# Kernel tuning notes

Measured on AMD Instinct MI355X. Metric: run time of the kernel, lower is better.

Reference implementation:

```python
import jax, jax.numpy as jnp
import numpy as np
import math

B, C, IMG, E, H, L, FF, D, NCLS = 4, 3, 64, 256, 8, 512, 4, 4, 1000
N = IMG * IMG  # 4096 pixel tokens
HS = H * E    # head_size = embedding_size * heads (per original code)


def setup_inputs() -> dict:
    key = jax.random.key(0)
    ks = jax.random.split(key, 32)
    s = 0.02
    nrm = lambda k, shape: (jax.random.normal(k, shape, jnp.float32) * s)
    inp = {
        "x": jax.random.normal(ks[0], (B, C, N), jnp.float32),
        "conv_w": nrm(ks[1], (E, C)),                 # 1x1 conv1d kernel
        "conv_b": jnp.zeros((E,), jnp.float32),
        "pos_emb": nrm(ks[2], (N, E)),
        "latents": jax.random.normal(ks[3], (L, E), jnp.float32),
        # cross-attention (queries from latents, keys/values from image tokens)
        "ca_wq": nrm(ks[4], (E, HS)),
        "ca_wk": nrm(ks[5], (E, HS)),
        "ca_wv": nrm(ks[6], (E, HS)),
        "ca_wu": nrm(ks[7], (HS, E)),
        "ca_bu": jnp.zeros((E,), jnp.float32),
        "ca_ln_g": jnp.ones((E,), jnp.float32),
        "ca_ln_b": jnp.zeros((E,), jnp.float32),
        # transformer blocks, stacked along depth for lax.scan
        "blk_wq": nrm(ks[8], (D, E, HS)),
        "blk_wk": nrm(ks[9], (D, E, HS)),
        "blk_wv": nrm(ks[10], (D, E, HS)),
        "blk_wu": nrm(ks[11], (D, HS, E)),
        "blk_bu": jnp.zeros((D, E), jnp.float32),
        "blk_ln1_g": jnp.ones((D, E), jnp.float32),
        "blk_ln1_b": jnp.zeros((D, E), jnp.float32),
        "blk_w1": nrm(ks[12], (D, E, FF * E)),
        "blk_b1": jnp.zeros((D, FF * E), jnp.float32),
        "blk_w2": nrm(ks[13], (D, FF * E, E)),
        "blk_b2": jnp.zeros((D, E), jnp.float32),
        "blk_ln2_g": jnp.ones((D, E), jnp.float32),
        "blk_ln2_b": jnp.zeros((D, E), jnp.float32),
        "cls_w": nrm(ks[14], (E, NCLS)),
        "cls_b": jnp.zeros((NCLS,), jnp.float32),
        "heads": H,
    }
    return inp


def _ln(x, g, b):
    m = jnp.mean(x, axis=-1, keepdims=True)
    v = jnp.mean(jnp.square(x - m), axis=-1, keepdims=True)
    return g * (x - m) * jax.lax.rsqrt(v + 1e-5) + b


def _mha(q_in, kv_in, wq, wk, wv, wu, bu, heads):
    # Faithful to original: each head has dim = embedding_size (head_size = heads*emb),
    # and the scale is sqrt(emb // heads).
    b, nq, e = q_in.shape
    nk = kv_in.shape[1]
    q = (q_in @ wq).reshape(b, nq, heads, e)
    k = (kv_in @ wk).reshape(b, nk, heads, e)
    v = (kv_in @ wv).reshape(b, nk, heads, e)
    scale = 1.0 / math.sqrt(e // heads)
    w = jax.nn.softmax(jnp.einsum('bqhe,bkhe->bhqk', q, k) * scale, axis=-1)
    a = jnp.einsum('bhqk,bkhe->bqhe', w, v).reshape(b, nq, heads * e)
    return a @ wu + bu


def reference(x, conv_w, conv_b, pos_emb, latents,
              ca_wq, ca_wk, ca_wv, ca_wu, ca_bu, ca_ln_g, ca_ln_b,
              blk_wq, blk_wk, blk_wv, blk_wu, blk_bu,
              blk_ln1_g, blk_ln1_b, blk_w1, blk_b1, blk_w2, blk_b2,
              blk_ln2_g, blk_ln2_b, cls_w, cls_b, heads):
    bsz = x.shape[0]
    # 1x1 conv1d over flattened pixels: (B, C, N) -> (B, N, E), plus positions
    tokens = jnp.einsum('bcn,ec->bne', x, conv_w) + conv_b + pos_emb
    # latents as queries, image tokens as keys/values (cross-attention)
    z = jnp.broadcast_to(latents, (bsz,) + latents.shape)
    z = _ln(_mha(z, tokens, ca_wq, ca_wk, ca_wv, ca_wu, ca_bu, heads) + z,
            ca_ln_g, ca_ln_b)
    # dropout is identity in eval mode

    def block(z, p):
        wq, wk, wv, wu, bu, g1, b1, w1, c1, w2, c2, g2, b2 = p
        z = _ln(_mha(z, z, wq, wk, wv, wu, bu, heads) + z, g1, b1)
        h = jax.nn.gelu(z @ w1 + c1, approximate=False) @ w2 + c2
        z = _ln(h + z, g2, b2)
        return z, None

    z, _ = jax.lax.scan(block, z,
                        (blk_wq, blk_wk, blk_wv, blk_wu, blk_bu,
                         blk_ln1_g, blk_ln1_b, blk_w1, blk_b1,
                         blk_w2, blk_b2, blk_ln2_g, blk_ln2_b))
    # global average over latents, then classifier
    return jnp.mean(z, axis=1) @ cls_w + cls_b
```

## Files before the change

kernel.cpp:

```cpp
#include <hip/hip_runtime.h>
#include <hip/hip_bf16.h>
#include <math.h>


typedef __attribute__((ext_vector_type(8))) short s8v;
typedef __attribute__((ext_vector_type(4))) float f32x4;
typedef __attribute__((ext_vector_type(16))) float f32x16;
typedef __attribute__((ext_vector_type(4))) unsigned u32x4;

__device__ __forceinline__ short f2b(float f) {
  union { float f; unsigned u; } a; a.f = f;
  unsigned r = a.u + 0x7fff + ((a.u >> 16) & 1);
  return (short)(r >> 16);
}
__device__ __forceinline__ float b2f(short s) {
  union { unsigned u; float f; } a; a.u = ((unsigned)(unsigned short)s) << 16;
  return a.f;
}
__device__ __forceinline__ unsigned cvtpk(float lo, float hi) {
  unsigned r;
  asm("v_cvt_pk_bf16_f32 %0, %1, %2" : "=v"(r) : "v"(lo), "v"(hi));
  return r;
}

__device__ __forceinline__ void gl16(const void* gp, void* lp) {
  __builtin_amdgcn_global_load_lds(
      (const __attribute__((address_space(1))) unsigned int*)gp,
      (__attribute__((address_space(3))) unsigned int*)lp, 16, 0, 0);
}

__global__ __launch_bounds__(256) void k_tokens(
    const float* __restrict__ x, const float* __restrict__ cw,
    const float* __restrict__ cb, const float* __restrict__ pe,
    short* __restrict__ tok)
{
  int idx = blockIdx.x * 256 + threadIdx.x;
  int e = idx & 255;
  int n = (idx >> 8) & 4095;
  int b = idx >> 20;
  float s = cb[e] + pe[n * 256 + e];
#pragma unroll
  for (int c = 0; c < 3; ++c)
    s += x[b * 12288 + c * 4096 + n] * cw[e * 3 + c];
  tok[idx] = f2b(s);
}

template<typename TI>
__global__ __launch_bounds__(256) void k_tr(
    const TI* __restrict__ in, short* __restrict__ out,
    int R, int C, long sIn, long sOut)
{
  __shared__ float t[32][33];
  const TI* ib = in + (long)blockIdx.z * sIn;
  short* ob = out + (long)blockIdx.z * sOut;
  int c0 = blockIdx.x * 32, r0 = blockIdx.y * 32;
  int tx = threadIdx.x & 31, ty = threadIdx.x >> 5;
#pragma unroll
  for (int i = 0; i < 4; ++i)
    t[ty * 4 + i][tx] = (float)ib[(long)(r0 + ty * 4 + i) * C + c0 + tx];
  __syncthreads();
#pragma unroll
  for (int i = 0; i < 4; ++i)
    ob[(long)(c0 + ty * 4 + i) * R + r0 + tx] = f2b(t[tx][ty * 4 + i]);
}

struct TrJob {
  const float* src; short* dst;
  int R, C; long sIn, sOut;
  int mode, tilesPerZ, z, tileBase;
  float scale;
};
struct TrJobs { TrJob j[11]; };

__global__ __launch_bounds__(256) void k_trbatch(TrJobs jb, int njobs)
{
  __shared__ float t[32][33];
  int tb = blockIdx.x, ji = 0;
#pragma unroll
  for (int k = 1; k < 11; ++k)
    if (k < njobs && tb >= jb.j[k].tileBase) ji = k;
  TrJob J = jb.j[ji];
  int local = tb - J.tileBase;
  if (J.mode == 1) {
    long o = (long)local * 8192 + threadIdx.x;
#pragma unroll
    for (int k = 0; k < 32; ++k)
      J.dst[o + k * 256] = f2b(J.src[o + k * 256] * J.scale);
    return;
  }
  int zi = local / J.tilesPerZ, ti = local - zi * J.tilesPerZ;
  int ntx = J.C >> 5;
  int tx = ti % ntx, ty = ti / ntx;
  const float* ib = J.src + (long)zi * J.sIn;
  short* ob = J.dst + (long)zi * J.sOut;
  int c0 = tx * 32, r0 = ty * 32;
  int lx = threadIdx.x & 31, ly = threadIdx.x >> 5;
#pragma unroll
  for (int i = 0; i < 4; ++i)
    t[ly * 4 + i][lx] = ib[(long)(r0 + ly * 4 + i) * J.C + c0 + lx];
  __syncthreads();
#pragma unroll
  for (int i = 0; i < 4; ++i)
    ob[(long)(c0 + ly * 4 + i) * J.R + r0 + lx] = f2b(t[lx][ly * 4 + i] * J.scale);
}

template<int EPI>
__global__ __launch_bounds__(256) void k_mgemm(
    const short* __restrict__ A, const short* __restrict__ Bt,
    void* __restrict__ Cv, const float* __restrict__ bias,
    int K, int lda, int ldb, int ldc,
    long sA, long sB, long sC, int zdA, int zmA, int zdB, int zmB)
{
  __shared__ char As[8192];
  __shared__ char Bs[8192];
  int z = blockIdx.z;
  const short* Ab = A + ((long)((z / zdA) % zmA)) * sA;
  const short* Bb = Bt + ((long)((z / zdB) % zmB)) * sB;
  int t = threadIdx.x;
  int lane = t & 63, w = t >> 6;
  int wr = w >> 1, wc = w & 1;
  int g = lane >> 4, l15 = lane & 15;
  long row0 = (long)blockIdx.y * 128, col0 = (long)blockIdx.x * 128;
  const f32x4 zz = {0.f, 0.f, 0.f, 0.f};
  f32x4 acc[4][4];
#pragma unroll
  for (int m = 0; m < 4; ++m)
#pragma unroll
    for (int n = 0; n < 4; ++n) acc[m][n] = zz;

  auto mload = [&](s8v* aa, s8v* bb, int kk) {
#pragma unroll
    for (int i = 0; i < 2; ++i) {
      int r = i * 64 + (t >> 2), c = t & 3;
      aa[i] = *(const s8v*)&Ab[(row0 + r) * (long)lda + kk + c * 8];
      bb[i] = *(const s8v*)&Bb[(col0 + r) * (long)ldb + kk + c * 8];
    }
  };
  auto mstore = [&](s8v* aa, s8v* bb) {
#pragma unroll
    for (int i = 0; i < 2; ++i) {
      int r = i * 64 + (t >> 2), c = t & 3;
      int off = (r * 64 + c * 16) ^ ((r & 7) << 4);
      *(s8v*)&As[off] = aa[i];
      *(s8v*)&Bs[off] = bb[i];
    }
  };
  auto mcomp = [&]() {
    s8v af[4], bfr[4];
#pragma unroll
    for (int m = 0; m < 4; ++m) {
      int r = wr * 64 + m * 16 + l15;
      af[m] = *(const s8v*)&As[(r * 64 + g * 16) ^ ((r & 7) << 4)];
    }
#pragma unroll
    for (int n = 0; n < 4; ++n) {
      int r = wc * 64 + n * 16 + l15;
      bfr[n] = *(const s8v*)&Bs[(r * 64 + g * 16) ^ ((r & 7) << 4)];
    }
#pragma unroll
    for (int m = 0; m < 4; ++m)
#pragma unroll
      for (int n = 0; n < 4; ++n)
        acc[m][n] = __builtin_amdgcn_mfma_f32_16x16x32_bf16(af[m], bfr[n], acc[m][n], 0, 0, 0);
  };

  s8v a0[2], b0[2], a1[2], b1[2];
  mload(a0, b0, 0);
  for (int k0 = 0; k0 < K; k0 += 64) {
    __syncthreads(); mstore(a0, b0); __syncthreads();
    mload(a1, b1, k0 + 32);
    mcomp();
    __syncthreads(); mstore(a1, b1); __syncthreads();
    if (k0 + 64 < K) mload(a0, b0, k0 + 64);
    mcomp();
  }

  long zo = (long)z * sC;
#pragma unroll
  for (int m = 0; m < 4; ++m)
#pragma unroll
    for (int n = 0; n < 4; ++n)
#pragma unroll
      for (int r = 0; r < 4; ++r) {
        long rr = row0 + wr * 64 + m * 16 + g * 4 + r;
        long cc = col0 + wc * 64 + n * 16 + l15;
        float v = acc[m][n][r];
        if (EPI == 1) {
          v += bias[cc];
          v = 0.5f * v * (1.f + erff(v * 0.70710678118654752f));
        }
        if (EPI == 2)
          ((float*)Cv)[zo + rr * ldc + cc] = v;
        else
          ((short*)Cv)[zo + rr * ldc + cc] = f2b(v);
      }
}

__global__ __launch_bounds__(512, 2) void k_mflash5(
    const short* __restrict__ Qp, const short* __restrict__ Kp,
    const short* __restrict__ Vtp, short* __restrict__ Opart,
    float* __restrict__ MLp,
    int nk, int ldq, int ldk, int ldvt,
    long qh, long qb, long kh, long kb, long vh, long vb)
{
  __shared__ char pool[131072];
  int t = threadIdx.x, lane = t & 63, w = t >> 6;
  int l31 = lane & 31, hi = lane >> 5;
  int h = blockIdx.y, b = blockIdx.z;
  int kv = blockIdx.x & 3, qblk = blockIdx.x >> 2;
  const short* Q  = Qp  + (long)h * qh + (long)b * qb;
  const short* Kg = Kp  + (long)h * kh + (long)b * kb;
  const short* Vg = Vtp + (long)h * vh + (long)b * vb;
  int q0w = qblk * 256 + w * 32;
  int nkq = nk >> 2;
  int NIT = nkq >> 6;
  long k0 = (long)kv * nkq;

  s8v qf[16];
  {
    const short* Qrow = Q + (long)(q0w + l31) * ldq + hi * 8;
#pragma unroll
    for (int s = 0; s < 16; ++s) qf[s] = *(const s8v*)(Qrow + s * 16);
  }

  const char* KgB = (const char*)Kg;
  const char* VgB = (const char*)Vg;
  unsigned koff[4], voff[4];
#pragma unroll
  for (int c = 0; c < 4; ++c) {
    int r = 8 * w + 2 * c + hi;
    koff[c] = (unsigned)((k0 + r) * (long)ldk * 2) + ((l31 ^ (r & 31)) << 4);
    int rv = 32 * w + 8 * c + (lane >> 3);
    voff[c] = (unsigned)(((long)rv * ldvt + k0) * 2) + (((lane & 7) ^ (lane >> 3)) << 4);
  }
  const unsigned kStep = (unsigned)(64 * ldk * 2);

  auto stage = [&](int bsel) {
    char* kd = pool + bsel * 65536 + (w << 12);
    char* vd = kd + 32768;
#pragma unroll
    for (int c = 0; c < 4; ++c) { gl16(KgB + koff[c], kd + c * 1024); koff[c] += kStep; }
#pragma unroll
    for (int c = 0; c < 4; ++c) { gl16(VgB + voff[c], vd + c * 1024); voff[c] += 128; }
  };

  f32x16 accO[8];
#pragma unroll
  for (int n = 0; n < 8; ++n)
#pragma unroll
    for (int i = 0; i < 16; ++i) accO[n][i] = 0.f;
  float mrow = -1e30f, lrow = 0.f;

  stage(0);

  for (int it = 0; it < NIT; ++it) {
    int cur = it & 1;
    asm volatile("s_waitcnt vmcnt(0)" ::: "memory");
    __syncthreads();
    if (it + 1 < NIT) stage(cur ^ 1);
    const char* kls = pool + cur * 65536;
    const char* vls = kls + 32768;

    f32x16 sacc[2];
#pragma unroll
    for (int i = 0; i < 16; ++i) { sacc[0][i] = 0.f; sacc[1][i] = 0.f; }
    __builtin_amdgcn_s_setprio(1);
#pragma unroll
    for (int tt = 0; tt < 2; ++tt) {
      int r = tt * 32 + l31;
#pragma unroll
      for (int s = 0; s < 16; ++s) {
        s8v kf = *(const s8v*)&kls[r * 512 + (((2 * s + hi) ^ l31) << 4)];
        sacc[tt] = __builtin_amdgcn_mfma_f32_32x32x16_bf16(kf, qf[s], sacc[tt], 0, 0, 0);
      }
    }
    __builtin_amdgcn_s_setprio(0);

    float mt = sacc[0][0];
#pragma unroll
    for (int i = 1; i < 16; ++i) mt = fmaxf(mt, sacc[0][i]);
#pragma unroll
    for (int i = 0; i < 16; ++i) mt = fmaxf(mt, sacc[1][i]);
    mt = fmaxf(mt, __shfl_xor(mt, 32));
    if (__any(mt - mrow > 8.f)) {
      float mn = fmaxf(mrow, mt);
      float al = __expf(mrow - mn);
      mrow = mn; lrow *= al;
#pragma unroll
      for (int r = 0; r < 16; ++r) {
        float alr = __shfl(al, (r & 3) + 8 * (r >> 2) + 4 * hi);
#pragma unroll
        for (int n = 0; n < 8; ++n) accO[n][r] *= alr;
      }
    }
    float ls = 0.f;
#pragma unroll
    for (int tt = 0; tt < 2; ++tt)
#pragma unroll
      for (int i = 0; i < 16; ++i) {
        float p = __expf(sacc[tt][i] - mrow);
        sacc[tt][i] = p; ls += p;
      }
    ls += __shfl_xor(ls, 32);
    lrow += ls;

    s8v pa[4];
#pragma unroll
    for (int s = 0; s < 4; ++s) {
      int tt = s >> 1, r0 = (s & 1) * 8;
      unsigned w0 = cvtpk(sacc[tt][r0 + 0], sacc[tt][r0 + 1]);
      unsigned w1 = cvtpk(sacc[tt][r0 + 2], sacc[tt][r0 + 3]);
      unsigned w2 = cvtpk(sacc[tt][r0 + 4], sacc[tt][r0 + 5]);
      unsigned w3 = cvtpk(sacc[tt][r0 + 6], sacc[tt][r0 + 7]);
      unsigned x0 = (unsigned)__shfl_xor((int)w0, 32);
      unsigned x1 = (unsigned)__shfl_xor((int)w1, 32);
      unsigned x2 = (unsigned)__shfl_xor((int)w2, 32);
      unsigned x3 = (unsigned)__shfl_xor((int)w3, 32);
      u32x4 pw;
      pw.x = hi ? x2 : w0;
      pw.y = hi ? x3 : w1;
      pw.z = hi ? w2 : x0;
      pw.w = hi ? w3 : x1;
      pa[s] = *(s8v*)&pw;
    }

    __builtin_amdgcn_s_setprio(1);
#pragma unroll
    for (int n = 0; n < 8; ++n) {
      int rv = n * 32 + l31;
#pragma unroll
      for (int s2 = 0; s2 < 4; ++s2) {
        s8v vf = *(const s8v*)&vls[rv * 128 + (((2 * s2 + hi) ^ (l31 & 7)) << 4)];
        accO[n] = __builtin_amdgcn_mfma_f32_32x32x16_bf16(pa[s2], vf, accO[n], 0, 0, 0);
      }
    }
    __builtin_amdgcn_s_setprio(0);
  }

  long prow = (((long)kv * 4 + b) * 8 + h) * 512;
  short* Ob = Opart + prow * 256;
  float* MLb = MLp + prow * 2;
  if (lane < 32) {
    MLb[(q0w + l31) * 2] = mrow;
    MLb[(q0w + l31) * 2 + 1] = lrow;
  }
#pragma unroll
  for (int n = 0; n < 8; ++n)
#pragma unroll
    for (int r = 0; r < 16; ++r) {
      int q = q0w + (r & 3) + 8 * (r >> 2) + 4 * hi;
      Ob[(long)q * 256 + n * 32 + l31] = f2b(accO[n][r]);
    }
}

__global__ __launch_bounds__(512) void k_fcomb(
    const short* __restrict__ Op, const float* __restrict__ ML,
    short* __restrict__ O)
{
  int d = threadIdx.x & 255;
  int q = blockIdx.x * 2 + (threadIdx.x >> 8);
  int h = blockIdx.y, b = blockIdx.z;
  const long kvs = 4L * 8 * 512;
  long r0 = ((long)b * 8 + h) * 512 + q;
  float mm[4], ll[4], m = -1e30f;
#pragma unroll
  for (int kv = 0; kv < 4; ++kv) {
    mm[kv] = ML[(kv * kvs + r0) * 2];
    ll[kv] = ML[(kv * kvs + r0) * 2 + 1];
    m = fmaxf(m, mm[kv]);
  }
  float wv[4], lsum = 0.f;
#pragma unroll
  for (int kv = 0; kv < 4; ++kv) { wv[kv] = __expf(mm[kv] - m); lsum += ll[kv] * wv[kv]; }
  float inv = 1.f / lsum, acc = 0.f;
#pragma unroll
  for (int kv = 0; kv < 4; ++kv)
    acc += b2f(Op[(kv * kvs + r0) * 256 + d]) * wv[kv];
  O[(long)b * 1048576 + (long)q * 2048 + h * 256 + d] = f2b(acc * inv);
}

__global__ __launch_bounds__(256) void k_bias_res_ln(
    const float* __restrict__ Yp, int nPart, long pStride,
    const float* __restrict__ bias,
    const float* __restrict__ res, int resMod,
    const float* __restrict__ g, const float* __restrict__ bta,
    float* __restrict__ out, short* __restrict__ out_bf)
{
  __shared__ float red[4];
  int row = blockIdx.x, e = threadIdx.x;
  float v = bias[e] + res[(long)(row % resMod) * 256 + e];
  for (int s = 0; s < nPart; ++s) v += Yp[s * pStride + (long)row * 256 + e];
  float s1 = v;
#pragma unroll
  for (int o = 32; o > 0; o >>= 1) s1 += __shfl_down(s1, o);
  if ((e & 63) == 0) red[e >> 6] = s1;
  __syncthreads();
  float mean = (red[0] + red[1] + red[2] + red[3]) * (1.f / 256.f);
  float d = v - mean;
  __syncthreads();
  float s2 = d * d;
#pragma unroll
  for (int o = 32; o > 0; o >>= 1) s2 += __shfl_down(s2, o);
  if ((e & 63) == 0) red[e >> 6] = s2;
  __syncthreads();
  float var = (red[0] + red[1] + red[2] + red[3]) * (1.f / 256.f);
  float o = g[e] * d * rsqrtf(var + 1e-5f) + bta[e];
  out[(long)row * 256 + e] = o;
  out_bf[(long)row * 256 + e] = f2b(o);
}

__global__ __launch_bounds__(256) void k_meancls(
    const float* __restrict__ z, const float* __restrict__ w,
    const float* __restrict__ bias, float* __restrict__ out)
{
  __shared__ float zms[256];
  int b = blockIdx.y, e = threadIdx.x;
  float s = 0.f;
  for (int l = 0; l < 512; ++l) s += z[((long)b * 512 + l) * 256 + e];
  zms[e] = s * (1.f / 512.f);
  __syncthreads();
  int j = blockIdx.x * 256 + e;
  if (j >= 1000) return;
  float acc = bias[j];
  for (int e2 = 0; e2 < 256; ++e2) acc += zms[e2] * w[e2 * 1000 + j];
  out[b * 1000 + j] = acc;
}

extern "C" void kernel_launch(void* const* d_in, const int* in_sizes, int n_in,
                              void* d_out, int out_size, void* d_ws, size_t ws_size,
                              hipStream_t stream)
{
  (void)in_sizes; (void)n_in; (void)out_size; (void)ws_size;
  const float* x       = (const float*)d_in[0];
  const float* conv_w  = (const float*)d_in[1];
  const float* conv_b  = (const float*)d_in[2];
  const float* pos_emb = (const float*)d_in[3];
  const float* latents = (const float*)d_in[4];
  const float* ca_wq   = (const float*)d_in[5];
  const float* ca_wk   = (const float*)d_in[6];
  const float* ca_wv   = (const float*)d_in[7];
  const float* ca_wu   = (const float*)d_in[8];
  const float* ca_bu   = (const float*)d_in[9];
  const float* ca_ln_g = (const float*)d_in[10];
  const float* ca_ln_b = (const float*)d_in[11];
  const float* blk_wq  = (const float*)d_in[12];
  const float* blk_wk  = (const float*)d_in[13];
  const float* blk_wv  = (const float*)d_in[14];
  const float* blk_wu  = (const float*)d_in[15];
  const float* blk_bu  = (const float*)d_in[16];
  const float* blk_ln1_g = (const float*)d_in[17];
  const float* blk_ln1_b = (const float*)d_in[18];
  const float* blk_w1  = (const float*)d_in[19];
  const float* blk_b1  = (const float*)d_in[20];
  const float* blk_w2  = (const float*)d_in[21];
  const float* blk_b2  = (const float*)d_in[22];
  const float* blk_ln2_g = (const float*)d_in[23];
  const float* blk_ln2_b = (const float*)d_in[24];
  const float* cls_w   = (const float*)d_in[25];
  const float* cls_b   = (const float*)d_in[26];
  float* out = (float*)d_out;

  short* wqT_ca = (short*)d_ws;
  short* wkT_ca = wqT_ca + 524288;
  short* wuT_ca = wkT_ca + 524288;
  short* wv_ca  = wuT_ca + 524288;
  short* lat_bf = wv_ca + 524288;
  short* wqkT   = lat_bf + 131072;
  short* wvT    = wqkT + 4194304;
  short* wuT_b  = wvT + 2097152;
  short* w1T    = wuT_b + 2097152;
  short* w2T    = w1T + 1048576;
  short* tok_bf = w2T + 1048576;
  short* tokT   = tok_bf + 4194304;
  short* qCA    = tokT + 4194304;
  short* qtil   = qCA + 1048576;
  short* MstT   = qtil + 1048576;
  short* VtB    = MstT + 524288;
  short* bufO   = VtB + 4194304;
  short* h1     = bufO + 4194304;
  short* z_bf   = h1 + 2097152;
  float* z      = (float*)(z_bf + 524288);
  float* zm     = z + 524288;
  float* Ypart  = zm + 1024;
  short* Opart  = (short*)(Ypart + 4194304);
  float* MLp    = (float*)(Opart + 16777216);
  short* QKb    = tok_bf;

  const float scale = 0.17677669529663687f;
  const int BIG = 1 << 30;

  TrJobs JB; int nj = 0, base = 0;
  auto addT = [&](const float* s, short* d, int R, int C, long sIn, long sOut,
                  int zc, float sc) {
    int tpz = (C >> 5) * (R >> 5);
    JB.j[nj] = {s, d, R, C, sIn, sOut, 0, tpz, zc, base, sc};
    base += tpz * zc; ++nj;
  };
  auto addC = [&](const float* s, short* d, int nelem) {
    int tpz = nelem >> 13;
    JB.j[nj] = {s, d, 0, 0, 0, 0, 1, tpz, 1, base, 1.f};
    base += tpz; ++nj;
  };
  addT(ca_wq, wqT_ca, 256, 2048, 0, 0, 1, scale);
  addT(ca_wk, wkT_ca, 256, 2048, 0, 0, 1, 1.f);
  addT(ca_wu, wuT_ca, 2048, 256, 0, 0, 1, 1.f);
  addT(blk_wq, wqkT, 256, 2048, 524288, 1048576, 4, scale);
  addT(blk_wk, wqkT + 524288, 256, 2048, 524288, 1048576, 4, 1.f);
  addT(blk_wv, wvT, 256, 2048, 524288, 524288, 4, 1.f);
  addT(blk_wu, wuT_b, 2048, 256, 524288, 524288, 4, 1.f);
  addT(blk_w1, w1T, 256, 1024, 262144, 262144, 4, 1.f);
  addT(blk_w2, w2T, 1024, 256, 262144, 262144, 4, 1.f);
  addC(ca_wv, wv_ca, 524288);
  addC(latents, lat_bf, 131072);
  k_trbatch<<<base, 256, 0, stream>>>(JB, nj);

  k_tokens<<<16384, 256, 0, stream>>>(x, conv_w, conv_b, pos_emb, tok_bf);
  k_tr<__hip_bfloat16><<<dim3(8, 128, 4), 256, 0, stream>>>(
      (const __hip_bfloat16*)tok_bf, tokT, 4096, 256, 1048576, 1048576);

  k_mgemm<0><<<dim3(16, 4, 1), 256, 0, stream>>>(
      lat_bf, wqT_ca, qCA, nullptr, 256, 256, 256, 2048, 0, 0, 0, 1, BIG, 1, BIG);
  k_mgemm<0><<<dim3(2, 4, 8), 256, 0, stream>>>(
      qCA, wkT_ca, qtil, nullptr, 256, 2048, 256, 256, 256, 65536, 131072, 1, 8, 1, 8);
  k_mgemm<0><<<dim3(2, 2, 8), 256, 0, stream>>>(
      wuT_ca, wv_ca, MstT, nullptr, 256, 2048, 2048, 2048, 256, 256, 256, 1, 8, 1, 8);
  k_mflash5<<<dim3(8, 8, 4), 512, 0, stream>>>(
      qtil, tok_bf, tokT, Opart, MLp, 4096, 256, 256, 4096,
      131072L, 0L, 0L, 1048576L, 0L, 1048576L);
  k_fcomb<<<dim3(256, 8, 4), 512, 0, stream>>>(Opart, MLp, bufO);
  k_mgemm<2><<<dim3(2, 16, 8), 256, 0, stream>>>(
      bufO, MstT, Ypart, nullptr, 256, 2048, 2048, 256, 256, 256, 524288, 1, 8, 1, 8);
  k_bias_res_ln<<<2048, 256, 0, stream>>>(Ypart, 8, 524288L, ca_bu, latents, 512,
                                          ca_ln_g, ca_ln_b, z, z_bf);

  for (int d = 0; d < 4; ++d) {
    k_mgemm<0><<<dim3(32, 16, 1), 256, 0, stream>>>(
        z_bf, wqkT + (long)d * 1048576, QKb, nullptr,
        256, 256, 256, 4096, 0, 0, 0, 1, BIG, 1, BIG);
    k_mgemm<0><<<dim3(4, 2, 32), 256, 0, stream>>>(
        wvT + (long)d * 524288, z_bf, VtB, nullptr,
        256, 256, 256, 512, 65536, 131072, 131072, 1, 8, 8, BIG);
    k_mflash5<<<dim3(8, 8, 4), 512, 0, stream>>>(
        QKb, QKb + 2048, VtB, Opart, MLp, 512, 4096, 4096, 512,
        256L, 2097152L, 256L, 2097152L, 131072L, 1048576L);
    k_fcomb<<<dim3(256, 8, 4), 512, 0, stream>>>(Opart, MLp, bufO);
    k_mgemm<2><<<dim3(2, 16, 8), 256, 0, stream>>>(
        bufO, wuT_b + (long)d * 524288, Ypart, nullptr,
        256, 2048, 2048, 256, 256, 256, 524288, 1, 8, 1, 8);
    k_bias_res_ln<<<2048, 256, 0, stream>>>(Ypart, 8, 524288L, blk_bu + d * 256, z, 2048,
        blk_ln1_g + d * 256, blk_ln1_b + d * 256, z, z_bf);
    k_mgemm<1><<<dim3(8, 16, 1), 256, 0, stream>>>(
        z_bf, w1T + (long)d * 262144, h1, blk_b1 + d * 1024,
        256, 256, 256, 1024, 0, 0, 0, 1, BIG, 1, BIG);
    k_mgemm<2><<<dim3(2, 16, 8), 256, 0, stream>>>(
        h1, w2T + (long)d * 262144, Ypart, nullptr,
        128, 1024, 1024, 256, 128, 128, 524288, 1, 8, 1, 8);
    k_bias_res_ln<<<2048, 256, 0, stream>>>(Ypart, 8, 524288L, blk_b2 + d * 256, z, 2048,
        blk_ln2_g + d * 256, blk_ln2_b + d * 256, z, z_bf);
  }

  k_meancls<<<dim3(4, 4), 256, 0, stream>>>(z, cls_w, cls_b, out);
}
```

Before: 635.7 us.

## Fuse token embedding with transpose and vectorize flash partial-output stores

Token embedding and its transpose now happen in one kernel: each thread computes 32 consecutive pixels for one channel, writes the row-major token and a vectorized 16-byte transposed store. This removes one kernel launch and the re-read of the token buffer for transposition. The flash attention epilogue stages the accumulator through a free LDS buffer so each lane can write 16-byte contiguous bf16 chunks instead of scattered 2-byte stores. In exchange, the row-major token stores in the new kernel are 2-byte strided per thread, though still coalesced across the block, and the epilogue adds LDS traffic.

```diff
diff --git a/kernel.cpp b/kernel.cpp
--- a/kernel.cpp
+++ b/kernel.cpp
@@ -29,39 +29,28 @@
       (__attribute__((address_space(3))) unsigned int*)lp, 16, 0, 0);
 }
 
-__global__ __launch_bounds__(256) void k_tokens(
+__global__ __launch_bounds__(256) void k_tokens2(
     const float* __restrict__ x, const float* __restrict__ cw,
     const float* __restrict__ cb, const float* __restrict__ pe,
-    short* __restrict__ tok)
-{
-  int idx = blockIdx.x * 256 + threadIdx.x;
-  int e = idx & 255;
-  int n = (idx >> 8) & 4095;
-  int b = idx >> 20;
-  float s = cb[e] + pe[n * 256 + e];
-#pragma unroll
-  for (int c = 0; c < 3; ++c)
-    s += x[b * 12288 + c * 4096 + n] * cw[e * 3 + c];
-  tok[idx] = f2b(s);
-}
-
-template<typename TI>
-__global__ __launch_bounds__(256) void k_tr(
-    const TI* __restrict__ in, short* __restrict__ out,
-    int R, int C, long sIn, long sOut)
-{
-  __shared__ float t[32][33];
-  const TI* ib = in + (long)blockIdx.z * sIn;
-  short* ob = out + (long)blockIdx.z * sOut;
-  int c0 = blockIdx.x * 32, r0 = blockIdx.y * 32;
-  int tx = threadIdx.x & 31, ty = threadIdx.x >> 5;
+    short* __restrict__ tok, short* __restrict__ tokT)
+{
+  int b = blockIdx.y, n0 = blockIdx.x * 32;
+  int e = threadIdx.x;
+  float c0 = cw[e * 3], c1 = cw[e * 3 + 1], c2 = cw[e * 3 + 2], cbv = cb[e];
+  const float* xb = x + b * 12288 + n0;
+  short acc[32];
+#pragma unroll
+  for (int i = 0; i < 32; ++i) {
+    int n = n0 + i;
+    float s = cbv + pe[n * 256 + e] + xb[i] * c0 + xb[4096 + i] * c1 + xb[8192 + i] * c2;
+    short v = f2b(s);
+    tok[((long)b * 4096 + n) * 256 + e] = v;
+    acc[i] = v;
+  }
+  short* tr = tokT + ((long)b * 256 + e) * 4096 + n0;
 #pragma unroll
   for (int i = 0; i < 4; ++i)
-    t[ty * 4 + i][tx] = (float)ib[(long)(r0 + ty * 4 + i) * C + c0 + tx];
-  __syncthreads();
-#pragma unroll
-  for (int i = 0; i < 4; ++i)
-    ob[(long)(c0 + ty * 4 + i) * R + r0 + tx] = f2b(t[tx][ty * 4 + i]);
+    *reinterpret_cast<s8v*>(tr + i * 8) = *reinterpret_cast<s8v*>(acc + i * 8);
 }
 
 struct TrJob {
@@ -196,7 +185,7 @@
       }
 }
 
-__global__ __launch_bounds__(512, 2) void k_mflash5(
+__global__ __launch_bounds__(512, 2) void k_mflash8(
     const short* __restrict__ Qp, const short* __restrict__ Kp,
     const short* __restrict__ Vtp, short* __restrict__ Opart,
     float* __restrict__ MLp,
@@ -344,13 +333,27 @@
     MLb[(q0w + l31) * 2] = mrow;
     MLb[(q0w + l31) * 2 + 1] = lrow;
   }
-#pragma unroll
-  for (int n = 0; n < 8; ++n)
+  char* freebuf = pool + ((((NIT - 1) & 1) ^ 1) << 16);
+  float* st = (float*)(freebuf + w * 4096);
+  int orow = lane >> 1, ohalf = lane & 1;
+#pragma unroll
+  for (int n = 0; n < 8; ++n) {
 #pragma unroll
     for (int r = 0; r < 16; ++r) {
-      int q = q0w + (r & 3) + 8 * (r >> 2) + 4 * hi;
-      Ob[(long)q * 256 + n * 32 + l31] = f2b(accO[n][r]);
-    }
+      int ql = (r & 3) + 8 * (r >> 2) + 4 * hi;
+      st[ql * 32 + l31] = accO[n][r];
+    }
+    short obuf[16];
+#pragma unroll
+    for (int jj = 0; jj < 4; ++jj) {
+      f32x4 v = *(const f32x4*)&st[orow * 32 + ohalf * 16 + jj * 4];
+      obuf[jj * 4 + 0] = f2b(v.x); obuf[jj * 4 + 1] = f2b(v.y);
+      obuf[jj * 4 + 2] = f2b(v.z); obuf[jj * 4 + 3] = f2b(v.w);
+    }
+    short* dst = Ob + (long)(q0w + orow) * 256 + n * 32 + ohalf * 16;
+    *(s8v*)(dst) = *(s8v*)&obuf[0];
+    *(s8v*)(dst + 8) = *(s8v*)&obuf[8];
+  }
 }
 
 __global__ __launch_bounds__(512) void k_fcomb(
@@ -514,9 +517,8 @@
   addC(latents, lat_bf, 131072);
   k_trbatch<<<base, 256, 0, stream>>>(JB, nj);
 
-  k_tokens<<<16384, 256, 0, stream>>>(x, conv_w, conv_b, pos_emb, tok_bf);
-  k_tr<__hip_bfloat16><<<dim3(8, 128, 4), 256, 0, stream>>>(
-      (const __hip_bfloat16*)tok_bf, tokT, 4096, 256, 1048576, 1048576);
+  k_tokens2<<<dim3(128, 4), 256, 0, stream>>>(x, conv_w, conv_b, pos_emb,
+                                              tok_bf, tokT);
 
   k_mgemm<0><<<dim3(16, 4, 1), 256, 0, stream>>>(
       lat_bf, wqT_ca, qCA, nullptr, 256, 256, 256, 2048, 0, 0, 0, 1, BIG, 1, BIG);
@@ -524,7 +526,7 @@
       qCA, wkT_ca, qtil, nullptr, 256, 2048, 256, 256, 256, 65536, 131072, 1, 8, 1, 8);
   k_mgemm<0><<<dim3(2, 2, 8), 256, 0, stream>>>(
       wuT_ca, wv_ca, MstT, nullptr, 256, 2048, 2048, 2048, 256, 256, 256, 1, 8, 1, 8);
-  k_mflash5<<<dim3(8, 8, 4), 512, 0, stream>>>(
+  k_mflash8<<<dim3(8, 8, 4), 512, 0, stream>>>(
       qtil, tok_bf, tokT, Opart, MLp, 4096, 256, 256, 4096,
       131072L, 0L, 0L, 1048576L, 0L, 1048576L);
   k_fcomb<<<dim3(256, 8, 4), 512, 0, stream>>>(Opart, MLp, bufO);
@@ -540,7 +542,7 @@
     k_mgemm<0><<<dim3(4, 2, 32), 256, 0, stream>>>(
         wvT + (long)d * 524288, z_bf, VtB, nullptr,
         256, 256, 256, 512, 65536, 131072, 131072, 1, 8, 8, BIG);
-    k_mflash5<<<dim3(8, 8, 4), 512, 0, stream>>>(
+    k_mflash8<<<dim3(8, 8, 4), 512, 0, stream>>>(
         QKb, QKb + 2048, VtB, Opart, MLp, 512, 4096, 4096, 512,
         256L, 2097152L, 256L, 2097152L, 131072L, 1048576L);
     k_fcomb<<<dim3(256, 8, 4), 512, 0, stream>>>(Opart, MLp, bufO);
```

Result: no change. 639.5 us (+0.6%).
